# Performance work log

Hardware: AMD Instinct MI355X
Metric: run time of the kernel (lower is better)

## Reference

```python
import jax, jax.numpy as jnp
import numpy as np

HIDDEN = 1024
FFN = 2048
N_EXPERTS = 8
TOP_K = 2
BSZ, Q_LEN = 1, 2048


def setup_inputs() -> dict:
    key = jax.random.key(0)
    ks = jax.random.split(key, 8)
    T = BSZ * Q_LEN
    x = jax.random.normal(ks[0], (BSZ, Q_LEN, HIDDEN), dtype=jnp.float32)
    weights = jax.random.uniform(ks[1], (T, N_EXPERTS), dtype=jnp.float32)
    top_weights = jax.random.uniform(ks[2], (T, TOP_K), dtype=jnp.float32)
    top_experts = jax.random.randint(ks[3], (T, TOP_K), 0, N_EXPERTS, dtype=jnp.int64)
    s = 0.02
    w_up = jax.random.normal(ks[4], (N_EXPERTS, HIDDEN, FFN), dtype=jnp.float32) * s
    w_gate = jax.random.normal(ks[5], (N_EXPERTS, HIDDEN, FFN), dtype=jnp.float32) * s
    w_down = jax.random.normal(ks[6], (N_EXPERTS, FFN, HIDDEN), dtype=jnp.float32) * s
    return {"x": x, "weights": weights, "top_weights": top_weights,
            "top_experts": top_experts, "w_up": w_up, "w_gate": w_gate, "w_down": w_down}


def reference(x, weights, top_weights, top_experts, w_up, w_gate, w_down):
    # x: [B, S, H]; top_experts/top_weights: [T, K]; weights unused (parity with torch forward)
    B, S, H = x.shape
    E = w_up.shape[0]
    xf = x.reshape(-1, H)  # [T, H]
    # per-token combine weight for each expert: w_tok[t, e] = sum_k top_weights[t,k] * (top_experts[t,k]==e)
    onehot = jax.nn.one_hot(top_experts, E, dtype=x.dtype)  # [T, K, E]
    w_tok = jnp.einsum('tke,tk->te', onehot, top_weights)   # [T, E]

    def body(acc, ws):
        wu, wg, wd, we = ws  # [H,F], [H,F], [F,H], [T]
        h = jax.nn.silu(xf @ wu) * (xf @ wg)  # SwiGLU: act(up) * gate
        return acc + (h @ wd) * we[:, None], None

    out, _ = jax.lax.scan(body, jnp.zeros_like(xf), (w_up, w_gate, w_down, w_tok.T))
    return out.reshape(B, S, H)
```

## Files before the change

### kernel.cpp

```cpp
#include <hip/hip_runtime.h>
#include <hip/hip_bf16.h>
#include <stdint.h>

#define T_TOK 2048
#define HID   1024
#define FFN_  2048
#define NEXP  8
#define NPAIR 4096
#define MAXTILE 40
#define EXPELEM ((size_t)HID * FFN_)
#define NSLICE 16
#define NGEMM (MAXTILE * (FFN_ / 64))

typedef __bf16 bf16;
typedef __bf16 bf16x8 __attribute__((ext_vector_type(8)));
typedef __bf16 bf16x4 __attribute__((ext_vector_type(4)));
typedef float  f32x4  __attribute__((ext_vector_type(4)));
typedef float  f32x4v __attribute__((ext_vector_type(4)));
typedef unsigned int u32;

#define OFF_EXP   0
#define OFF_NT    64
#define OFF_TTE   128
#define OFF_TTM   512
#define OFF_TOK   1024
#define OFF_WGT   (OFF_TOK + 16384)
#define OFF_XG    65536
#define OFF_H1    (OFF_XG + (size_t)NPAIR*HID*2)
#define OFF_WT    (OFF_H1 + (size_t)NPAIR*FFN_*2)

__device__ __forceinline__ void gld16(const void* g, void* l) {
    __builtin_amdgcn_global_load_lds(
        (const __attribute__((address_space(1))) u32*)g,
        (__attribute__((address_space(3))) u32*)l, 16, 0, 0);
}

__global__ void __launch_bounds__(1024)
route_kernel(const uint32_t* __restrict__ te_raw,
             const float* __restrict__ top_w,
             int* __restrict__ expert_off,
             int* __restrict__ ntile_g,
             int* __restrict__ tte, int* __restrict__ ttm,
             int* __restrict__ tok, float* __restrict__ wgt)
{
    __shared__ int cnt[NSLICE][NEXP];
    __shared__ int off[NSLICE][NEXP];
    __shared__ int ebase[NEXP + 1];
    __shared__ int is64_s;
    int tid = threadIdx.x;
    int wv = tid >> 6, lane = tid & 63;

    if (wv == 0) {
        int bad = (te_raw[2 * lane + 1] != 0u);
        unsigned long long m = __ballot(bad);
        if (lane == 0) is64_s = (m == 0ull);
    }
    __syncthreads();
    int is64 = is64_s;

    int c[NEXP] = {0,0,0,0,0,0,0,0};
    int eids[4];
    #pragma unroll
    for (int it = 0; it < 4; ++it) {
        int p = wv * 256 + it * 64 + lane;
        int eid = is64 ? (int)te_raw[2*p] : (int)te_raw[p];
        eids[it] = eid;
        #pragma unroll
        for (int e = 0; e < NEXP; ++e) {
            unsigned long long m = __ballot(eid == e);
            c[e] += __popcll(m);
        }
    }
    if (lane == 0)
        #pragma unroll
        for (int e = 0; e < NEXP; ++e) cnt[wv][e] = c[e];
    __syncthreads();

    if (tid < NEXP) {
        int run = 0;
        for (int s = 0; s < NSLICE; ++s) { off[s][tid] = run; run += cnt[s][tid]; }
        ebase[tid] = run;
    }
    __syncthreads();
    if (tid == 0) {
        int s = 0;
        for (int e = 0; e < NEXP; ++e) { int t = ebase[e]; ebase[e] = s; expert_off[e] = s; s += t; }
        ebase[NEXP] = s; expert_off[NEXP] = s;
        int nt = 0;
        for (int e = 0; e < NEXP; ++e)
            for (int m = ebase[e]; m < ebase[e + 1]; m += 128) { tte[nt] = e; ttm[nt] = m; ++nt; }
        *ntile_g = nt;
    }
    __syncthreads();

    int roff[NEXP];
    #pragma unroll
    for (int e = 0; e < NEXP; ++e) roff[e] = ebase[e] + off[wv][e];
    #pragma unroll
    for (int it = 0; it < 4; ++it) {
        int p = wv * 256 + it * 64 + lane;
        int eid = eids[it];
        int dest = -1;
        #pragma unroll
        for (int e = 0; e < NEXP; ++e) {
            unsigned long long m = __ballot(eid == e);
            if (eid == e) dest = roff[e] + __popcll(m & ((1ull << lane) - 1ull));
            roff[e] += __popcll(m);
        }
        tok[dest] = p >> 1;
        wgt[dest] = top_w[p];
    }
}

__global__ void gather_kernel(const float* __restrict__ x,
                              const int* __restrict__ tok,
                              bf16* __restrict__ Xg)
{
    int p = blockIdx.x;
    int t = tok[p];
    const float4* src = (const float4*)(x + (size_t)t * HID);
    float4 v = src[threadIdx.x];
    bf16x4 o;
    o[0] = (bf16)v.x; o[1] = (bf16)v.y; o[2] = (bf16)v.z; o[3] = (bf16)v.w;
    *(bf16x4*)(Xg + (size_t)p * HID + threadIdx.x * 4) = o;
}

__global__ void __launch_bounds__(256)
transpose_v5(const float* __restrict__ in1, bf16* __restrict__ out1,
             const float* __restrict__ in2, bf16* __restrict__ out2,
             int nz1, int R, int C)
{
    __shared__ u32 tile32[4][64 * 32];
    int z = blockIdx.z;
    const float* in = (z < nz1) ? in1 : in2;
    bf16* o         = (z < nz1) ? out1 : out2;
    int e = (z < nz1) ? z : z - nz1;
    in += (size_t)e * R * C;
    o  += (size_t)e * R * C;
    int kt = blockIdx.x, nq = blockIdx.y;
    int k0 = kt * 64, c0 = nq * 256;
    int tid = threadIdx.x;
    int rbase = tid >> 6;
    int c4 = tid & 63;
    int grp = c4 >> 4, cq = c4 & 15;
    int fp0 = cq * 2;
    const float* base = in + (size_t)(k0 + rbase) * C + c0 + c4 * 4;
    f32x4v rb[16];
    #pragma unroll
    for (int it = 0; it < 16; ++it)
        rb[it] = __builtin_nontemporal_load((const f32x4v*)(base + (size_t)it * 4 * C));
    #pragma unroll
    for (int it = 0; it < 16; ++it) {
        int r = rbase + it * 4;
        union { bf16 h[2]; u32 w; } a, b;
        a.h[0] = (bf16)rb[it][0]; a.h[1] = (bf16)rb[it][1];
        b.h[0] = (bf16)rb[it][2]; b.h[1] = (bf16)rb[it][3];
        tile32[grp][r * 32 + (fp0       ^ (r & 31))] = a.w;
        tile32[grp][r * 32 + ((fp0 + 1) ^ (r & 31))] = b.w;
    }
    __syncthreads();
    int RT = R >> 6;
    #pragma unroll
    for (int it2 = 0; it2 < 8; ++it2) {
        int gg = it2 * 256 + tid;
        int group = gg >> 9, g = gg & 511;
        int f = g >> 3;
        int k8 = ((g & 7) ^ (f & 7)) * 8;
        union { bf16 h[8]; } pk;
        #pragma unroll
        for (int j = 0; j < 8; ++j) {
            u32 u = tile32[group][(k8 + j) * 32 + ((f >> 1) ^ ((k8 + j) & 31))];
            pk.h[j] = (f & 1) ? ((bf16*)&u)[1] : ((bf16*)&u)[0];
        }
        bf16* tbase = o + ((size_t)(nq * 4 + group) * RT + kt) * 4096;
        *(bf16x8*)(tbase + (size_t)g * 8) = *(bf16x8*)&pk;
    }
}

__global__ void __launch_bounds__(256)
fused_ug(const bf16* __restrict__ Xg,
         const bf16* __restrict__ wuT, const bf16* __restrict__ wgT,
         const int* __restrict__ expert_off, const int* __restrict__ ntile_g,
         const int* __restrict__ tte, const int* __restrict__ ttm,
         int eb, int gcnt, bf16* __restrict__ H1,
         const float* __restrict__ tin1, bf16* __restrict__ tout1,
         const float* __restrict__ tin2, bf16* __restrict__ tout2,
         int tnz1, int tR, int tC)
{
    __shared__ char ldsbuf[32768];
    int bid = blockIdx.x;
    int tid = threadIdx.x;

    if (bid >= NGEMM) {
        u32 (*tile32)[64 * 32] = (u32 (*)[64 * 32])ldsbuf;
        int tb = bid - NGEMM;
        int nkt = tR >> 6;
        int perslice = nkt * (tC >> 8);
        int z = tb / perslice, rem = tb - z * perslice;
        int kt = rem % nkt, nq = rem / nkt;
        const float* in; bf16* o; int e2;
        if (z < tnz1) { in = tin1; o = tout1; e2 = z; }
        else          { in = tin2; o = tout2; e2 = z - tnz1; }
        in += (size_t)e2 * tR * tC;
        o  += (size_t)e2 * tR * tC;
        int k0 = kt * 64, c0 = nq * 256;
        int rbase = tid >> 6;
        int c4 = tid & 63;
        int grp = c4 >> 4, cq = c4 & 15;
        int fp0 = cq * 2;
        const float* base = in + (size_t)(k0 + rbase) * tC + c0 + c4 * 4;
        f32x4v rb[16];
        #pragma unroll
        for (int it = 0; it < 16; ++it)
            rb[it] = __builtin_nontemporal_load((const f32x4v*)(base + (size_t)it * 4 * tC));
        #pragma unroll
        for (int it = 0; it < 16; ++it) {
            int r = rbase + it * 4;
            union { bf16 h[2]; u32 w; } a, b;
            a.h[0] = (bf16)rb[it][0]; a.h[1] = (bf16)rb[it][1];
            b.h[0] = (bf16)rb[it][2]; b.h[1] = (bf16)rb[it][3];
            tile32[grp][r * 32 + (fp0       ^ (r & 31))] = a.w;
            tile32[grp][r * 32 + ((fp0 + 1) ^ (r & 31))] = b.w;
        }
        __syncthreads();
        #pragma unroll
        for (int it2 = 0; it2 < 8; ++it2) {
            int gg = it2 * 256 + tid;
            int group = gg >> 9, g = gg & 511;
            int f = g >> 3;
            int k8 = ((g & 7) ^ (f & 7)) * 8;
            union { bf16 h[8]; } pk;
            #pragma unroll
            for (int j = 0; j < 8; ++j) {
                u32 u = tile32[group][(k8 + j) * 32 + ((f >> 1) ^ ((k8 + j) & 31))];
                pk.h[j] = (f & 1) ? ((bf16*)&u)[1] : ((bf16*)&u)[0];
            }
            bf16* tbase = o + ((size_t)(nq * 4 + group) * nkt + kt) * 4096;
            *(bf16x8*)(tbase + (size_t)g * 8) = *(bf16x8*)&pk;
        }
        return;
    }

    int ty = bid >> 5, bn = bid & 31;
    if (ty >= *ntile_g) return;
    int e = tte[ty];
    if (e < eb || e >= eb + gcnt) return;
    int m0 = ttm[ty];
    int p1 = expert_off[e + 1];
    int n0 = bn * 64;
    bf16* As  = (bf16*)ldsbuf;
    bf16* Bus = (bf16*)(ldsbuf + 16384);
    bf16* Bgs = (bf16*)(ldsbuf + 24576);
    int lane = tid & 63, wv = tid >> 6;
    int wm = wv >> 1, wn = wv & 1;
    int l16 = lane & 15, lhi = lane >> 4;
    f32x4 accU[4][2] = {};
    f32x4 accG[4][2] = {};

    const bf16* aptr[4]; u32 alds[4];
    #pragma unroll
    for (int c = 0; c < 4; ++c) {
        int g = c * 256 + tid;
        int r = g >> 3, pos = g & 7;
        int gr = m0 + r; if (gr >= p1) gr = p1 - 1;
        int gsrc = pos ^ (r & 7);
        aptr[c] = Xg + (size_t)gr * HID + gsrc * 8;
        alds[c] = g * 16;
    }
    size_t tb0 = (size_t)e * EXPELEM + (size_t)(n0 >> 6) * (HID >> 6) * 4096;
    const bf16* buptr[2]; const bf16* bgptr[2]; u32 blds[2];
    #pragma unroll
    for (int c = 0; c < 2; ++c) {
        int g = c * 256 + tid;
        buptr[c] = wuT + tb0 + (size_t)g * 8;
        bgptr[c] = wgT + tb0 + (size_t)g * 8;
        blds[c] = g * 16;
    }
    u32 aro[2][4], bro[2][2];
    #pragma unroll
    for (int ks = 0; ks < 2; ++ks) {
        #pragma unroll
        for (int fm = 0; fm < 4; ++fm) {
            int r = wm * 64 + fm * 16 + l16;
            aro[ks][fm] = r * 128 + ((u32)((ks * 4 + lhi) ^ (r & 7))) * 16;
        }
        #pragma unroll
        for (int fn = 0; fn < 2; ++fn) {
            int fr = wn * 32 + fn * 16 + l16;
            bro[ks][fn] = fr * 128 + ((u32)((ks * 4 + lhi) ^ (fr & 7))) * 16;
        }
    }

    for (int t = 0; t < HID / 64; ++t) {
        #pragma unroll
        for (int c = 0; c < 4; ++c) { gld16(aptr[c], (char*)As + alds[c]); aptr[c] += 64; }
        #pragma unroll
        for (int c = 0; c < 2; ++c) {
            gld16(buptr[c], (char*)Bus + blds[c]); buptr[c] += 4096;
            gld16(bgptr[c], (char*)Bgs + blds[c]); bgptr[c] += 4096;
        }
        __syncthreads();
        #pragma unroll
        for (int ks = 0; ks < 2; ++ks) {
            bf16x8 af[4];
            #pragma unroll
            for (int fm = 0; fm < 4; ++fm)
                af[fm] = *(const bf16x8*)((char*)As + aro[ks][fm]);
            #pragma unroll
            for (int fn = 0; fn < 2; ++fn) {
                bf16x8 bu = *(const bf16x8*)((char*)Bus + bro[ks][fn]);
                bf16x8 bg = *(const bf16x8*)((char*)Bgs + bro[ks][fn]);
                #pragma unroll
                for (int fm = 0; fm < 4; ++fm) {
                    accU[fm][fn] = __builtin_amdgcn_mfma_f32_16x16x32_bf16(af[fm], bu, accU[fm][fn], 0, 0, 0);
                    accG[fm][fn] = __builtin_amdgcn_mfma_f32_16x16x32_bf16(af[fm], bg, accG[fm][fn], 0, 0, 0);
                }
            }
        }
        __syncthreads();
    }
    #pragma unroll
    for (int fm = 0; fm < 4; ++fm)
    #pragma unroll
    for (int fn = 0; fn < 2; ++fn)
    #pragma unroll
    for (int rg = 0; rg < 4; ++rg) {
        int r = m0 + wm * 64 + fm * 16 + lhi * 4 + rg;
        if (r < p1) {
            float u = accU[fm][fn][rg], g = accG[fm][fn][rg];
            float h = (u / (1.f + __expf(-u))) * g;
            int fc = n0 + wn * 32 + fn * 16 + l16;
            H1[(size_t)r * FFN_ + fc] = (bf16)h;
        }
    }
}

__global__ void __launch_bounds__(256)
moe_down(const bf16* __restrict__ H1, const bf16* __restrict__ wdT,
         const int* __restrict__ expert_off, const int* __restrict__ ntile_g,
         const int* __restrict__ tte, const int* __restrict__ ttm,
         const int* __restrict__ tok, const float* __restrict__ wgt,
         float* __restrict__ out)
{
    int ty = blockIdx.y;
    if (ty >= *ntile_g) return;
    int e = tte[ty];
    int m0 = ttm[ty];
    int p1 = expert_off[e + 1];
    int n0 = blockIdx.x * 64;
    __shared__ bf16 As[128 * 64];
    __shared__ bf16 Bs [64 * 64];
    __shared__ float wgt_s[128];
    __shared__ int   tok_s[128];
    int tid = threadIdx.x, lane = tid & 63, wv = tid >> 6;
    int wm = wv >> 1, wn = wv & 1;
    int l16 = lane & 15, lhi = lane >> 4;
    if (tid < 128) {
        int r = m0 + tid;
        if (r < p1) { wgt_s[tid] = wgt[r]; tok_s[tid] = tok[r]; }
        else        { wgt_s[tid] = 0.f;    tok_s[tid] = 0; }
    }
    f32x4 acc[4][2] = {};

    const bf16* aptr[4]; u32 alds[4];
    #pragma unroll
    for (int c = 0; c < 4; ++c) {
        int g = c * 256 + tid;
        int r = g >> 3, pos = g & 7;
        int gr = m0 + r; if (gr >= p1) gr = p1 - 1;
        int gsrc = pos ^ (r & 7);
        aptr[c] = H1 + (size_t)gr * FFN_ + gsrc * 8;
        alds[c] = g * 16;
    }
    size_t tb0 = (size_t)e * EXPELEM + (size_t)(n0 >> 6) * (FFN_ >> 6) * 4096;
    const bf16* bptr[2]; u32 blds[2];
    #pragma unroll
    for (int c = 0; c < 2; ++c) {
        int g = c * 256 + tid;
        bptr[c] = wdT + tb0 + (size_t)g * 8;
        blds[c] = g * 16;
    }
    u32 aro[2][4], bro[2][2];
    #pragma unroll
    for (int ks = 0; ks < 2; ++ks) {
        #pragma unroll
        for (int fm = 0; fm < 4; ++fm) {
            int r = wm * 64 + fm * 16 + l16;
            aro[ks][fm] = r * 128 + ((u32)((ks * 4 + lhi) ^ (r & 7))) * 16;
        }
        #pragma unroll
        for (int fn = 0; fn < 2; ++fn) {
            int fr = wn * 32 + fn * 16 + l16;
            bro[ks][fn] = fr * 128 + ((u32)((ks * 4 + lhi) ^ (fr & 7))) * 16;
        }
    }

    for (int t = 0; t < FFN_ / 64; ++t) {
        #pragma unroll
        for (int c = 0; c < 4; ++c) { gld16(aptr[c], (char*)As + alds[c]); aptr[c] += 64; }
        #pragma unroll
        for (int c = 0; c < 2; ++c) { gld16(bptr[c], (char*)Bs + blds[c]); bptr[c] += 4096; }
        __syncthreads();
        #pragma unroll
        for (int ks = 0; ks < 2; ++ks) {
            bf16x8 af[4];
            #pragma unroll
            for (int fm = 0; fm < 4; ++fm)
                af[fm] = *(const bf16x8*)((char*)As + aro[ks][fm]);
            #pragma unroll
            for (int fn = 0; fn < 2; ++fn) {
                bf16x8 bd = *(const bf16x8*)((char*)Bs + bro[ks][fn]);
                #pragma unroll
                for (int fm = 0; fm < 4; ++fm)
                    acc[fm][fn] = __builtin_amdgcn_mfma_f32_16x16x32_bf16(af[fm], bd, acc[fm][fn], 0, 0, 0);
            }
        }
        __syncthreads();
    }
    #pragma unroll
    for (int fm = 0; fm < 4; ++fm)
    #pragma unroll
    for (int fn = 0; fn < 2; ++fn)
    #pragma unroll
    for (int rg = 0; rg < 4; ++rg) {
        int rl = wm * 64 + fm * 16 + lhi * 4 + rg;
        if (m0 + rl < p1) {
            float v = acc[fm][fn][rg] * wgt_s[rl];
            atomicAdd(out + (size_t)tok_s[rl] * HID + n0 + wn * 32 + fn * 16 + l16, v);
        }
    }
}

extern "C" void kernel_launch(void* const* d_in, const int* in_sizes, int n_in,
                              void* d_out, int out_size, void* d_ws, size_t ws_size,
                              hipStream_t stream)
{
    const float*    x      = (const float*)d_in[0];
    const float*    top_w  = (const float*)d_in[2];
    const uint32_t* te     = (const uint32_t*)d_in[3];
    const float*    w_up   = (const float*)d_in[4];
    const float*    w_gate = (const float*)d_in[5];
    const float*    w_down = (const float*)d_in[6];
    float* out = (float*)d_out;
    char*  ws  = (char*)d_ws;

    int*   expert_off = (int*)(ws + OFF_EXP);
    int*   ntile_g    = (int*)(ws + OFF_NT);
    int*   tte        = (int*)(ws + OFF_TTE);
    int*   ttm        = (int*)(ws + OFF_TTM);
    int*   tok        = (int*)(ws + OFF_TOK);
    float* wgt        = (float*)(ws + OFF_WGT);
    bf16*  Xg         = (bf16*)(ws + OFF_XG);
    bf16*  H1         = (bf16*)(ws + OFF_H1);
    bf16*  WT         = (bf16*)(ws + OFF_WT);
    bf16*  wuT = WT;
    bf16*  wgT = WT + 8 * EXPELEM;
    bf16*  wdT = WT + 16 * EXPELEM;

    hipMemsetAsync(out, 0, (size_t)out_size * sizeof(float), stream);
    hipLaunchKernelGGL(route_kernel, dim3(1), dim3(1024), 0, stream,
                       te, top_w, expert_off, ntile_g, tte, ttm, tok, wgt);
    hipLaunchKernelGGL(gather_kernel, dim3(NPAIR), dim3(256), 0, stream,
                       x, tok, Xg);

    hipLaunchKernelGGL(transpose_v5, dim3(HID / 64, FFN_ / 256, 8), dim3(256), 0, stream,
                       w_up, wuT, w_gate, wgT, 4, HID, FFN_);

    hipLaunchKernelGGL(fused_ug, dim3(NGEMM + 1024), dim3(256), 0, stream,
                       Xg, wuT, wgT, expert_off, ntile_g, tte, ttm, 0, 4, H1,
                       w_up + 4 * EXPELEM, wuT + 4 * EXPELEM,
                       w_gate + 4 * EXPELEM, wgT + 4 * EXPELEM, 4, HID, FFN_);

    hipLaunchKernelGGL(fused_ug, dim3(NGEMM + 1024), dim3(256), 0, stream,
                       Xg, wuT, wgT, expert_off, ntile_g, tte, ttm, 4, 4, H1,
                       w_down, wdT, w_down, wdT, 8, FFN_, HID);

    hipLaunchKernelGGL(moe_down, dim3(HID / 64, MAXTILE), dim3(256), 0, stream,
                       H1, wdT, expert_off, ntile_g, tte, ttm, tok, wgt, out);
}
```

Before: 154.4 us.

## Split moe_down K loop across two 256-thread groups with LDS reduction

Doubles the moe_down block to 512 threads and splits the FFN reduction dimension into two halves, each handled by its own group of four waves with separate LDS staging buffers. Each half runs half the K iterations, then partial accumulators are combined through LDS before one group issues the weighted atomic adds. The goal is more waves per tile to hide memory latency and shorten the serial K loop of the down projection. The cost is more LDS per block, extra barriers and a reduction step, and possibly lower occupancy from the larger block.

Measured after the change: 162.1 us. +4.9%, slower.

```diff
diff --git a/kernel.cpp b/kernel.cpp
--- a/kernel.cpp
+++ b/kernel.cpp
@@ -335,7 +335,7 @@
     }
 }
 
-__global__ void __launch_bounds__(256)
+__global__ void __launch_bounds__(512)
 moe_down(const bf16* __restrict__ H1, const bf16* __restrict__ wdT,
          const int* __restrict__ expert_off, const int* __restrict__ ntile_g,
          const int* __restrict__ tte, const int* __restrict__ ttm,
@@ -348,12 +348,16 @@
     int m0 = ttm[ty];
     int p1 = expert_off[e + 1];
     int n0 = blockIdx.x * 64;
-    __shared__ bf16 As[128 * 64];
-    __shared__ bf16 Bs [64 * 64];
+    __shared__ char lds[49152];
     __shared__ float wgt_s[128];
     __shared__ int   tok_s[128];
-    int tid = threadIdx.x, lane = tid & 63, wv = tid >> 6;
-    int wm = wv >> 1, wn = wv & 1;
+    int tid = threadIdx.x;
+    int kg = tid >> 8;
+    int tid2 = tid & 255;
+    bf16* As = (bf16*)(lds + kg * 16384);
+    bf16* Bs = (bf16*)(lds + 32768 + kg * 8192);
+    int lane = tid2 & 63, wv2 = tid2 >> 6;
+    int wm = wv2 >> 1, wn = wv2 & 1;
     int l16 = lane & 15, lhi = lane >> 4;
     if (tid < 128) {
         int r = m0 + tid;
@@ -365,18 +369,19 @@
     const bf16* aptr[4]; u32 alds[4];
     #pragma unroll
     for (int c = 0; c < 4; ++c) {
-        int g = c * 256 + tid;
+        int g = c * 256 + tid2;
         int r = g >> 3, pos = g & 7;
         int gr = m0 + r; if (gr >= p1) gr = p1 - 1;
         int gsrc = pos ^ (r & 7);
-        aptr[c] = H1 + (size_t)gr * FFN_ + gsrc * 8;
+        aptr[c] = H1 + (size_t)gr * FFN_ + kg * (FFN_ / 2) + gsrc * 8;
         alds[c] = g * 16;
     }
-    size_t tb0 = (size_t)e * EXPELEM + (size_t)(n0 >> 6) * (FFN_ >> 6) * 4096;
+    size_t tb0 = (size_t)e * EXPELEM + (size_t)(n0 >> 6) * (FFN_ >> 6) * 4096
+               + (size_t)(kg * 16) * 4096;
     const bf16* bptr[2]; u32 blds[2];
     #pragma unroll
     for (int c = 0; c < 2; ++c) {
-        int g = c * 256 + tid;
+        int g = c * 256 + tid2;
         bptr[c] = wdT + tb0 + (size_t)g * 8;
         blds[c] = g * 16;
     }
@@ -395,7 +400,7 @@
         }
     }
 
-    for (int t = 0; t < FFN_ / 64; ++t) {
+    for (int t = 0; t < FFN_ / 128; ++t) {
         #pragma unroll
         for (int c = 0; c < 4; ++c) { gld16(aptr[c], (char*)As + alds[c]); aptr[c] += 64; }
         #pragma unroll
@@ -417,16 +422,40 @@
         }
         __syncthreads();
     }
-    #pragma unroll
-    for (int fm = 0; fm < 4; ++fm)
-    #pragma unroll
-    for (int fn = 0; fn < 2; ++fn)
-    #pragma unroll
-    for (int rg = 0; rg < 4; ++rg) {
-        int rl = wm * 64 + fm * 16 + lhi * 4 + rg;
-        if (m0 + rl < p1) {
-            float v = acc[fm][fn][rg] * wgt_s[rl];
-            atomicAdd(out + (size_t)tok_s[rl] * HID + n0 + wn * 32 + fn * 16 + l16, v);
+
+    float* xch = (float*)lds;
+    #pragma unroll
+    for (int fn = 0; fn < 2; ++fn) {
+        if (kg == 1) {
+            #pragma unroll
+            for (int fm = 0; fm < 4; ++fm)
+            #pragma unroll
+            for (int rg = 0; rg < 4; ++rg)
+                xch[(wm * 64 + fm * 16 + lhi * 4 + rg) * 32 + wn * 16 + l16] = acc[fm][fn][rg];
+        }
+        __syncthreads();
+        if (kg == 0) {
+            #pragma unroll
+            for (int fm = 0; fm < 4; ++fm)
+            #pragma unroll
+            for (int rg = 0; rg < 4; ++rg)
+                acc[fm][fn][rg] += xch[(wm * 64 + fm * 16 + lhi * 4 + rg) * 32 + wn * 16 + l16];
+        }
+        __syncthreads();
+    }
+
+    if (kg == 0) {
+        #pragma unroll
+        for (int fm = 0; fm < 4; ++fm)
+        #pragma unroll
+        for (int fn = 0; fn < 2; ++fn)
+        #pragma unroll
+        for (int rg = 0; rg < 4; ++rg) {
+            int rl = wm * 64 + fm * 16 + lhi * 4 + rg;
+            if (m0 + rl < p1) {
+                float v = acc[fm][fn][rg] * wgt_s[rl];
+                atomicAdd(out + (size_t)tok_s[rl] * HID + n0 + wn * 32 + fn * 16 + l16, v);
+            }
         }
     }
 }
@@ -475,6 +504,6 @@
                        Xg, wuT, wgT, expert_off, ntile_g, tte, ttm, 4, 4, H1,
                        w_down, wdT, w_down, wdT, 8, FFN_, HID);
 
-    hipLaunchKernelGGL(moe_down, dim3(HID / 64, MAXTILE), dim3(256), 0, stream,
+    hipLaunchKernelGGL(moe_down, dim3(HID / 64, MAXTILE), dim3(512), 0, stream,
                        H1, wdT, expert_off, ntile_g, tte, ttm, tok, wgt, out);
 }
```
